# Kernel optimization log

Hardware: AMD Instinct MI355X
Metric: run time of the kernel (lower is better)

## Reference

```python
import jax, jax.numpy as jnp
import numpy as np

# Static config
B, C, H, W = 1, 4, 64, 64
DIM, NH = 512, 16
HD = DIM // NH
SCALE = HD ** -0.5
WC, WH, WW = 2, 8, 8            # 3D window size
N = WC * WH * WW                # tokens per window = 128
SC, SH, SW = 1, 4, 4            # shift = window // 2
NWC, NWH, NWW = C // WC, H // WH, W // WW
NWIN = NWC * NWH * NWW          # windows per sample
HID = 4 * DIM
NBLK = 2                        # [no-shift, shift] pair


def _rel_idx():
    coords = np.stack(np.meshgrid(np.arange(WC), np.arange(WH), np.arange(WW), indexing='ij')).reshape(3, -1)
    rel = coords[:, :, None] - coords[:, None, :]
    rel[0] += WC - 1; rel[1] += WH - 1; rel[2] += WW - 1
    idx = rel[0] * (2 * WH - 1) * (2 * WW - 1) + rel[1] * (2 * WW - 1) + rel[2]
    return jnp.asarray(idx)  # [N, N] into 675-entry table

REL_IDX = _rel_idx()


def _shift_mask():
    img = np.zeros((C, H, W), np.int32)
    cnt = 0
    for cs in (slice(0, -WC), slice(-WC, -SC), slice(-SC, None)):
        for hs in (slice(0, -WH), slice(-WH, -SH), slice(-SH, None)):
            for ws in (slice(0, -WW), slice(-WW, -SW), slice(-SW, None)):
                img[cs, hs, ws] = cnt; cnt += 1
    img = img.reshape(NWC, WC, NWH, WH, NWW, WW).transpose(0, 2, 4, 1, 3, 5).reshape(NWIN, N)
    diff = img[:, :, None] != img[:, None, :]
    return jnp.asarray(np.where(diff, -100.0, 0.0).astype(np.float32))  # [NWIN, N, N]

MASK = _shift_mask()


def _win_part(x):  # [B,C,H,W,D] -> [B*NWIN, N, D]
    x = x.reshape(B, NWC, WC, NWH, WH, NWW, WW, DIM)
    return x.transpose(0, 1, 3, 5, 2, 4, 6, 7).reshape(B * NWIN, N, DIM)


def _win_rev(x):  # [B*NWIN, N, D] -> [B,C,H,W,D]
    x = x.reshape(B, NWC, NWH, NWW, WC, WH, WW, DIM)
    return x.transpose(0, 1, 4, 2, 5, 3, 6, 7).reshape(B, C, H, W, DIM)


def _ln(x, g, b):
    m = x.mean(-1, keepdims=True)
    v = ((x - m) ** 2).mean(-1, keepdims=True)
    return (x - m) / jnp.sqrt(v + 1e-5) * g + b


def _forward(x, ln1_g, ln1_b, qkv_w, qkv_b, bias_tab, proj_w, proj_b,
             ln2_g, ln2_b, fc1_w, fc1_b, fc2_w, fc2_b):
    for i in range(NBLK):
        shifted = (i % 2 == 1)
        shortcut = x
        h = _ln(x, ln1_g[i], ln1_b[i]).reshape(B, C, H, W, DIM)
        if shifted:
            h = jnp.roll(h, (-SC, -SH, -SW), axis=(1, 2, 3))
        xw = _win_part(h)  # [B*NWIN, N, DIM]
        qkv = (xw @ qkv_w[i] + qkv_b[i]).reshape(-1, N, 3, NH, HD).transpose(2, 0, 3, 1, 4)
        q, k, v = qkv[0] * SCALE, qkv[1], qkv[2]       # [B*NWIN, NH, N, HD]
        bias = bias_tab[i][REL_IDX].transpose(2, 0, 1)  # [NH, N, N]
        attn = jnp.einsum('whnd,whmd->whnm', q, k) + bias[None]
        if shifted:
            attn = (attn.reshape(B, NWIN, NH, N, N) + MASK[None, :, None]).reshape(-1, NH, N, N)
        attn = jax.nn.softmax(attn, axis=-1)
        out = jnp.einsum('whnm,whmd->wnhd', attn, v).reshape(-1, N, DIM)
        out = out @ proj_w[i] + proj_b[i]
        h = _win_rev(out)
        if shifted:
            h = jnp.roll(h, (SC, SH, SW), axis=(1, 2, 3))
        x = shortcut + h.reshape(B, C * H * W, DIM)
        h2 = _ln(x, ln2_g[i], ln2_b[i])
        h2 = jax.nn.gelu(h2 @ fc1_w[i] + fc1_b[i], approximate=False) @ fc2_w[i] + fc2_b[i]
        x = x + h2
    return x


def setup_inputs() -> dict:
    key = jax.random.key(0)
    ks = jax.random.split(key, 8)
    s = 0.02
    return {
        'x': jax.random.normal(ks[0], (B, C * H * W, DIM), jnp.float32),
        'ln1_g': jnp.ones((NBLK, DIM), jnp.float32),
        'ln1_b': jnp.zeros((NBLK, DIM), jnp.float32),
        'qkv_w': jax.random.normal(ks[1], (NBLK, DIM, 3 * DIM), jnp.float32) * s,
        'qkv_b': jnp.zeros((NBLK, 3 * DIM), jnp.float32),
        'bias_tab': jax.random.normal(ks[2], (NBLK, (2 * WC - 1) * (2 * WH - 1) * (2 * WW - 1), NH), jnp.float32) * s,
        'proj_w': jax.random.normal(ks[3], (NBLK, DIM, DIM), jnp.float32) * s,
        'proj_b': jnp.zeros((NBLK, DIM), jnp.float32),
        'ln2_g': jnp.ones((NBLK, DIM), jnp.float32),
        'ln2_b': jnp.zeros((NBLK, DIM), jnp.float32),
        'fc1_w': jax.random.normal(ks[4], (NBLK, DIM, HID), jnp.float32) * s,
        'fc1_b': jnp.zeros((NBLK, HID), jnp.float32),
        'fc2_w': jax.random.normal(ks[5], (NBLK, HID, DIM), jnp.float32) * s,
        'fc2_b': jnp.zeros((NBLK, DIM), jnp.float32),
    }


def reference(x, ln1_g, ln1_b, qkv_w, qkv_b, bias_tab, proj_w, proj_b,
              ln2_g, ln2_b, fc1_w, fc1_b, fc2_w, fc2_b):
    return _forward(x, ln1_g, ln1_b, qkv_w, qkv_b, bias_tab, proj_w, proj_b,
                    ln2_g, ln2_b, fc1_w, fc1_b, fc2_w, fc2_b)
```

## Files before the change

kernel.cpp:

```cpp
#include <hip/hip_runtime.h>
#include <stdint.h>

#define DIM 512
#define NHD 16
#define HD 32
#define NTOK 16384

typedef unsigned short u16;
typedef __attribute__((ext_vector_type(8))) short short8;
typedef __attribute__((ext_vector_type(4))) float f32x4;

__device__ __forceinline__ float bf2f(u16 u){ union{unsigned i; float f;} c; c.i=(unsigned)u<<16; return c.f; }
__device__ __forceinline__ float bflo(unsigned u){ union{unsigned i; float f;} c; c.i=u<<16; return c.f; }
__device__ __forceinline__ float bfhi(unsigned u){ union{unsigned i; float f;} c; c.i=u&0xffff0000u; return c.f; }
__device__ __forceinline__ u16 f2bf(float f){ union{float f; unsigned i;} c; c.f=f; unsigned r=(c.i + 0x7fffu + ((c.i>>16)&1u))>>16; return (u16)r; }

__device__ __forceinline__ int win_to_tok(int r, int shifted){
  int win = r >> 7, n = r & 127;
  int a = win >> 6, b = (win >> 3) & 7, c = win & 7;
  int ic = n >> 6, ih = (n >> 3) & 7, iw = n & 7;
  int gc = a*2 + ic, gh = b*8 + ih, gw = c*8 + iw;
  if (shifted){ gc = (gc + 1) & 3; gh = (gh + 4) & 63; gw = (gw + 4) & 63; }
  return (gc << 12) + (gh << 6) + gw;
}

__device__ __forceinline__ void gload16(const void* g, void* l){
  __builtin_amdgcn_global_load_lds(
    (const __attribute__((address_space(1))) unsigned int*)(unsigned long long)g,
    (__attribute__((address_space(3))) unsigned int*)(unsigned int)(unsigned long long)l,
    16, 0, 0);
}

__global__ __launch_bounds__(256)
void transpose_kernel(const float* __restrict__ W, u16* __restrict__ Wt, int K, int N)
{
  __shared__ float t[32][33];
  int n0 = blockIdx.x*32, k0 = blockIdx.y*32;
  int tx = threadIdx.x & 31, ty = threadIdx.x >> 5;
  #pragma unroll
  for (int i=0;i<4;i++) t[ty + i*8][tx] = W[(size_t)(k0 + ty + i*8)*N + n0 + tx];
  __syncthreads();
  #pragma unroll
  for (int i=0;i<4;i++) Wt[(size_t)(n0 + ty + i*8)*K + k0 + tx] = f2bf(t[tx][ty + i*8]);
}

__global__ __launch_bounds__(256)
void ln_kernel(const float* __restrict__ x, const float* __restrict__ g,
               const float* __restrict__ b, u16* __restrict__ out, int mode)
{
  int wave = threadIdx.x >> 6, lane = threadIdx.x & 63;
  int r = blockIdx.x * 4 + wave;
  int src = (mode < 0) ? r : win_to_tok(r, mode);
  const float4* xr = (const float4*)(x + (size_t)src * DIM);
  float4 v0 = xr[lane*2], v1 = xr[lane*2+1];
  float s  = v0.x+v0.y+v0.z+v0.w+v1.x+v1.y+v1.z+v1.w;
  float sq = v0.x*v0.x+v0.y*v0.y+v0.z*v0.z+v0.w*v0.w
           + v1.x*v1.x+v1.y*v1.y+v1.z*v1.z+v1.w*v1.w;
  #pragma unroll
  for (int o=32;o;o>>=1){ s += __shfl_xor(s,o); sq += __shfl_xor(sq,o); }
  float mean = s*(1.f/DIM);
  float var  = sq*(1.f/DIM) - mean*mean;
  float rstd = rsqrtf(var + 1e-5f);
  int c0 = lane*8;
  const float4* g4 = (const float4*)(g + c0);
  const float4* b4 = (const float4*)(b + c0);
  float4 ga = g4[0], gb = g4[1], ba = b4[0], bb = b4[1];
  float xv[8] = {v0.x,v0.y,v0.z,v0.w,v1.x,v1.y,v1.z,v1.w};
  float gg[8] = {ga.x,ga.y,ga.z,ga.w,gb.x,gb.y,gb.z,gb.w};
  float bv[8] = {ba.x,ba.y,ba.z,ba.w,bb.x,bb.y,bb.z,bb.w};
  union{u16 us[8]; uint4 u;} p;
  #pragma unroll
  for (int j=0;j<8;j++) p.us[j] = f2bf((xv[j]-mean)*rstd*gg[j] + bv[j]);
  ((uint4*)(out + (size_t)r*DIM))[lane] = p.u;
}

template<int EPI>
__global__ __launch_bounds__(256)
void gemm_kernel(const u16* __restrict__ X, const u16* __restrict__ Wt,
                 const float* __restrict__ bias, u16* __restrict__ obf,
                 float* __restrict__ xres, int M, int N, int K, int shifted)
{
  __shared__ u16 smem[4][128*64];
  int tid = threadIdx.x, wave = tid>>6, lane = tid&63;
  int nwg = gridDim.x * gridDim.y;
  int bid = blockIdx.y * gridDim.x + blockIdx.x;
  int wg  = (bid & 7) * (nwg >> 3) + (bid >> 3);
  int n0 = (wg % gridDim.x) * 128;
  int m0 = (wg / gridDim.x) * 128;
  int wm = (wave>>1)*64, wn = (wave&1)*64;
  f32x4 acc[4][4] = {};
  int srow = tid>>3;
  int soff = (((tid&7) ^ ((tid>>3)&7)))*8;

  auto stage = [&](int c, int k0){
    #pragma unroll
    for (int i=0;i<4;i++)
      gload16(X + (size_t)(m0 + i*32 + srow)*K + k0 + soff, (void*)(smem[c] + i*2048 + wave*512));
    #pragma unroll
    for (int i=0;i<4;i++)
      gload16(Wt + (size_t)(n0 + i*32 + srow)*K + k0 + soff, (void*)(smem[2+c] + i*2048 + wave*512));
  };

  stage(0, 0);
  __syncthreads();
  int nkt = K >> 6;
  for (int kt=0; kt<nkt; ++kt){
    int c = kt & 1;
    if (kt+1 < nkt) stage(c^1, (kt+1)<<6);
    const u16* Ab = smem[c];
    const u16* Bb = smem[2+c];
    #pragma unroll
    for (int kk=0; kk<64; kk+=32){
      short8 af[4], bfr[4];
      int cofs = (kk + (lane>>4)*8) ^ ((lane&7)<<3);
      #pragma unroll
      for (int mi=0;mi<4;mi++)
        af[mi] = *(const short8*)(Ab + (wm + mi*16 + (lane&15))*64 + cofs);
      #pragma unroll
      for (int nj=0;nj<4;nj++)
        bfr[nj] = *(const short8*)(Bb + (wn + nj*16 + (lane&15))*64 + cofs);
      __builtin_amdgcn_s_setprio(1);
      #pragma unroll
      for (int mi=0;mi<4;mi++)
        #pragma unroll
        for (int nj=0;nj<4;nj++)
          acc[mi][nj] = __builtin_amdgcn_mfma_f32_16x16x32_bf16(af[mi], bfr[nj], acc[mi][nj], 0,0,0);
      __builtin_amdgcn_s_setprio(0);
    }
    __syncthreads();
  }

  int lr = (lane>>4)*4, lc = lane&15;
  if (EPI==0 || EPI==2){
    u16* et = (u16*)smem;
    #pragma unroll
    for (int mi=0;mi<4;mi++){
      #pragma unroll
      for (int nj=0;nj<4;nj++){
        int col = wn + nj*16 + lc;
        float bv = bias[n0 + col];
        #pragma unroll
        for (int rr=0;rr<4;rr++){
          int row = wm + mi*16 + lr + rr;
          float v = acc[mi][nj][rr] + bv;
          if (EPI==2){
            float u2 = v*(1.5957691216057308f + 0.0713548162726f*v*v);
            v = v * __builtin_amdgcn_rcpf(1.f + __expf(-u2));
          }
          *(u16*)((char*)et + ((row*256 + col*2) ^ (((row>>2)&3)<<5))) = f2bf(v);
        }
      }
    }
    __syncthreads();
    #pragma unroll
    for (int j=0;j<8;j++){
      int q = j*256 + tid;
      int row = q>>4, cc = q&15;
      uint4 d = *(const uint4*)((char*)et + ((row*256 + cc*16) ^ (((row>>2)&3)<<5)));
      *(uint4*)(obf + (size_t)(m0+row)*N + n0 + cc*8) = d;
    }
  } else {
    float* et = (float*)smem;
    #pragma unroll
    for (int mi=0;mi<4;mi++){
      #pragma unroll
      for (int nj=0;nj<4;nj++){
        int col = wn + nj*16 + lc;
        float bv = bias[n0 + col];
        #pragma unroll
        for (int rr=0;rr<4;rr++){
          int row = wm + mi*16 + lr + rr;
          *(float*)((char*)et + ((row*512 + col*4) ^ (((row>>2)&1)<<6))) = acc[mi][nj][rr] + bv;
        }
      }
    }
    __syncthreads();
    #pragma unroll
    for (int j=0;j<16;j++){
      int q = j*256 + tid;
      int row = q>>5, cc = q&31;
      float4 d = *(const float4*)((char*)et + ((row*512 + cc*16) ^ (((row>>2)&1)<<6)));
      int grow = (EPI==1) ? win_to_tok(m0+row, shifted) : (m0+row);
      float4* p = (float4*)(xres + (size_t)grow*DIM + n0 + cc*4);
      float4 o = *p;
      o.x += d.x; o.y += d.y; o.z += d.z; o.w += d.w;
      *p = o;
    }
  }
}

__global__ __launch_bounds__(256)
void bias_kernel(const float* __restrict__ btab, float* __restrict__ biasM)
{
  int gid = blockIdx.x*256 + threadIdx.x;
  int q = (gid >> 7) & 127, k = gid & 127, h = gid >> 14;
  int ic=q>>6, ih=(q>>3)&7, iw=q&7, jc=k>>6, jh=(k>>3)&7, jw=k&7;
  int idx = (ic-jc+1)*225 + (ih-jh+7)*15 + (iw-jw+7);
  biasM[gid] = btab[idx*16 + h];
}

__global__ __launch_bounds__(256)
void attn_kernel(const u16* __restrict__ qkv, const float* __restrict__ biasM,
                 u16* __restrict__ out, int shifted)
{
  __shared__ u16 Ks[128*32];
  __shared__ u16 VsT[32*128];
  __shared__ u16 Ps[4][32*128];
  __shared__ int rid[128];
  int win = blockIdx.x >> 4, h = blockIdx.x & 15;
  int tid = threadIdx.x, wave = tid>>6, lane = tid&63;
  size_t base = (size_t)win*128*1536 + (size_t)h*32;

  {
    int m = tid>>1, half = tid&1;
    const uint4* ks = (const uint4*)(qkv + base + (size_t)m*1536 + 512 + half*16);
    uint4 k0v = ks[0], k1v = ks[1];
    char* krow = (char*)Ks + m*64;
    int c0 = half*32, sw = (m&3)<<4;
    *(uint4*)(krow + ((c0     ) ^ sw)) = k0v;
    *(uint4*)(krow + ((c0 + 16) ^ sw)) = k1v;
    const uint4* vs = (const uint4*)(qkv + base + (size_t)m*1536 + 1024 + half*16);
    union{u16 us[16]; uint4 u[2];} vv; vv.u[0]=vs[0]; vv.u[1]=vs[1];
    #pragma unroll
    for (int j=0;j<16;j++){
      int d = half*16 + j;
      *(u16*)((char*)VsT + ((d*256 + m*2) ^ ((d&7)<<4))) = vv.us[j];
    }
  }
  if (shifted && tid < 128){
    int a=win>>6, b=(win>>3)&7, c=win&7;
    int gc=a*2+(tid>>6), gh=b*8+((tid>>3)&7), gw=c*8+(tid&7);
    int rc = (gc<2)?0:((gc<3)?1:2);
    int rh = (gh<56)?0:((gh<60)?1:2);
    int rw = (gw<56)?0:((gw<60)?1:2);
    rid[tid] = rc*9 + rh*3 + rw;
  }
  __syncthreads();

  int q0 = wave*32;
  short8 qf[2];
  #pragma unroll
  for (int mi=0;mi<2;mi++){
    int ql = 16*mi + (lane&15);
    qf[mi] = *(const short8*)(qkv + base + (size_t)(q0+ql)*1536 + (lane>>4)*8);
  }
  f32x4 s[2][8] = {};
  #pragma unroll
  for (int nj=0;nj<8;nj++){
    int row = (lane&15) + 16*nj;
    short8 kf = *(const short8*)((char*)Ks + row*64 + ((((lane>>4)<<4)) ^ ((row&3)<<4)));
    #pragma unroll
    for (int mi=0;mi<2;mi++)
      s[mi][nj] = __builtin_amdgcn_mfma_f32_16x16x32_bf16(qf[mi], kf, s[mi][nj], 0,0,0);
  }

  int rk[8];
  if (shifted){
    #pragma unroll
    for (int nj=0;nj<8;nj++) rk[nj] = rid[(lane&15) + 16*nj];
  }
  float invl[2][4];
  char* pbase = (char*)Ps[wave];
  #pragma unroll
  for (int mi=0;mi<2;mi++){
    #pragma unroll
    for (int r=0;r<4;r++){
      int ql = 16*mi + ((lane>>4)<<2) + r;
      int qw = q0 + ql;
      const float* bp = biasM + (((h<<7) + qw)<<7) + (lane&15);
      int rq = shifted ? rid[qw] : 0;
      float sv[8]; float mx = -1e30f;
      #pragma unroll
      for (int nj=0;nj<8;nj++){
        float v = s[mi][nj][r] * 0.17677669529663687f + bp[nj*16];
        if (shifted && rk[nj] != rq) v -= 100.f;
        sv[nj] = v; mx = fmaxf(mx, v);
      }
      #pragma unroll
      for (int o=1;o<16;o<<=1) mx = fmaxf(mx, __shfl_xor(mx, o));
      float sum = 0.f;
      #pragma unroll
      for (int nj=0;nj<8;nj++){ float p = __expf(sv[nj]-mx); sv[nj]=p; sum += p; }
      #pragma unroll
      for (int o=1;o<16;o<<=1) sum += __shfl_xor(sum, o);
      invl[mi][r] = 1.f/sum;
      char* prow = pbase + ql*256;
      int sw = (ql&7)<<4;
      #pragma unroll
      for (int nj=0;nj<8;nj++)
        *(u16*)(prow + ((((lane&15) + (nj<<4))<<1) ^ sw)) = f2bf(sv[nj]);
    }
  }

  f32x4 o2[2][2] = {};
  #pragma unroll
  for (int kk=0;kk<4;kk++){
    int coff = kk*64 + ((lane>>4)<<4);
    short8 pa[2], vb[2];
    #pragma unroll
    for (int mi=0;mi<2;mi++){
      int ql = 16*mi + (lane&15);
      pa[mi] = *(const short8*)(pbase + ql*256 + (coff ^ ((ql&7)<<4)));
    }
    #pragma unroll
    for (int nj=0;nj<2;nj++){
      int d = (lane&15) + 16*nj;
      vb[nj] = *(const short8*)((char*)VsT + d*256 + (coff ^ ((d&7)<<4)));
    }
    #pragma unroll
    for (int mi=0;mi<2;mi++)
      #pragma unroll
      for (int nj=0;nj<2;nj++)
        o2[mi][nj] = __builtin_amdgcn_mfma_f32_16x16x32_bf16(pa[mi], vb[nj], o2[mi][nj], 0,0,0);
  }

  #pragma unroll
  for (int mi=0;mi<2;mi++){
    #pragma unroll
    for (int nj=0;nj<2;nj++){
      #pragma unroll
      for (int r=0;r<4;r++){
        int ql = 16*mi + ((lane>>4)<<2) + r;
        int d  = (lane&15) + (nj<<4);
        out[(size_t)(win*128 + q0 + ql)*DIM + (h<<5) + d] = f2bf(o2[mi][nj][r] * invl[mi][r]);
      }
    }
  }
}

extern "C" void kernel_launch(void* const* d_in, const int* in_sizes, int n_in,
                              void* d_out, int out_size, void* d_ws, size_t ws_size,
                              hipStream_t stream)
{
  const float* x_in   = (const float*)d_in[0];
  const float* ln1_g  = (const float*)d_in[1];
  const float* ln1_b  = (const float*)d_in[2];
  const float* qkv_w  = (const float*)d_in[3];
  const float* qkv_b  = (const float*)d_in[4];
  const float* btab   = (const float*)d_in[5];
  const float* proj_w = (const float*)d_in[6];
  const float* proj_b = (const float*)d_in[7];
  const float* ln2_g  = (const float*)d_in[8];
  const float* ln2_b  = (const float*)d_in[9];
  const float* fc1_w  = (const float*)d_in[10];
  const float* fc1_b  = (const float*)d_in[11];
  const float* fc2_w  = (const float*)d_in[12];
  const float* fc2_b  = (const float*)d_in[13];

  char* ws = (char*)d_ws;
  size_t off = 0;
  auto alloc = [&](size_t bytes)->char*{ char* p = ws + off; off += (bytes + 255) & ~(size_t)255; return p; };
  u16* wT_qkv = (u16*)alloc((size_t)2*512*1536*2);
  u16* wT_proj= (u16*)alloc((size_t)2*512*512*2);
  u16* wT_fc1 = (u16*)alloc((size_t)2*2048*512*2);
  u16* wT_fc2 = (u16*)alloc((size_t)2*512*2048*2);
  u16* bufA   = (u16*)alloc((size_t)16384*2048*2);
  u16* bufQ   = (u16*)alloc((size_t)16384*1536*2);
  u16* bufB   = (u16*)alloc((size_t)16384*512*2);
  float* biasM= (float*)alloc((size_t)16*128*128*4);
  (void)ws_size; (void)in_sizes; (void)n_in; (void)out_size;

  float* x = (float*)d_out;
  hipMemcpyAsync(x, x_in, (size_t)NTOK*DIM*4, hipMemcpyDeviceToDevice, stream);

  for (int i=0;i<2;i++){
    transpose_kernel<<<dim3(1536/32, 512/32), 256, 0, stream>>>(qkv_w + (size_t)i*512*1536, wT_qkv + (size_t)i*512*1536, 512, 1536);
    transpose_kernel<<<dim3( 512/32, 512/32), 256, 0, stream>>>(proj_w + (size_t)i*512*512,  wT_proj + (size_t)i*512*512,  512, 512);
    transpose_kernel<<<dim3(2048/32, 512/32), 256, 0, stream>>>(fc1_w + (size_t)i*512*2048, wT_fc1 + (size_t)i*2048*512, 512, 2048);
    transpose_kernel<<<dim3( 512/32,2048/32), 256, 0, stream>>>(fc2_w + (size_t)i*2048*512, wT_fc2 + (size_t)i*512*2048, 2048, 512);
  }

  for (int i=0;i<2;i++){
    ln_kernel<<<4096, 256, 0, stream>>>(x, ln1_g+i*512, ln1_b+i*512, bufA, i);
    gemm_kernel<0><<<dim3(12,128), 256, 0, stream>>>(bufA, wT_qkv+(size_t)i*512*1536, qkv_b+i*1536, bufQ, nullptr, NTOK,1536,512, 0);
    bias_kernel<<<1024, 256, 0, stream>>>(btab + (size_t)i*675*16, biasM);
    attn_kernel<<<2048, 256, 0, stream>>>(bufQ, biasM, bufB, i);
    gemm_kernel<1><<<dim3(4,128), 256, 0, stream>>>(bufB, wT_proj+(size_t)i*512*512, proj_b+i*512, nullptr, x, NTOK,512,512, i);
    ln_kernel<<<4096, 256, 0, stream>>>(x, ln2_g+i*512, ln2_b+i*512, bufB, -1);
    gemm_kernel<2><<<dim3(16,128), 256, 0, stream>>>(bufB, wT_fc1+(size_t)i*2048*512, fc1_b+i*2048, bufA, nullptr, NTOK,2048,512, 0);
    gemm_kernel<3><<<dim3(4,128), 256, 0, stream>>>(bufA, wT_fc2+(size_t)i*512*2048, fc2_b+i*512, nullptr, x, NTOK,512,2048, 0);
  }
}
```

Before: 435.8 us.

## Add K=32 GEMM variant with halved LDS for QKV, FC1 and FC2

Adds a gemm32 kernel that stages 32-wide K tiles instead of 64-wide ones. Shared memory drops from 64KB to 32KB, and the LDS layout gets a new XOR swizzle with two rows packed per 128-byte line. The fp32 residual epilogue is split into two 64-row halves so it fits in the smaller buffer. The aim is higher occupancy per CU for the QKV, FC1 and FC2 GEMMs, at the cost of twice as many barriers and K iterations.

```diff
diff --git a/kernel.cpp b/kernel.cpp
--- a/kernel.cpp
+++ b/kernel.cpp
@@ -76,11 +76,11 @@
 
 template<int EPI>
 __global__ __launch_bounds__(256)
-void gemm_kernel(const u16* __restrict__ X, const u16* __restrict__ Wt,
-                 const float* __restrict__ bias, u16* __restrict__ obf,
-                 float* __restrict__ xres, int M, int N, int K, int shifted)
-{
-  __shared__ u16 smem[4][128*64];
+void gemm32_kernel(const u16* __restrict__ X, const u16* __restrict__ Wt,
+                   const float* __restrict__ bias, u16* __restrict__ obf,
+                   float* __restrict__ xres, int M, int N, int K)
+{
+  __shared__ u16 smem[16384];
   int tid = threadIdx.x, wave = tid>>6, lane = tid&63;
   int nwg = gridDim.x * gridDim.y;
   int bid = blockIdx.y * gridDim.x + blockIdx.x;
@@ -89,50 +89,56 @@
   int m0 = (wg / gridDim.x) * 128;
   int wm = (wave>>1)*64, wn = (wave&1)*64;
   f32x4 acc[4][4] = {};
-  int srow = tid>>3;
-  int soff = (((tid&7) ^ ((tid>>3)&7)))*8;
-
-  auto stage = [&](int c, int k0){
-    #pragma unroll
-    for (int i=0;i<4;i++)
-      gload16(X + (size_t)(m0 + i*32 + srow)*K + k0 + soff, (void*)(smem[c] + i*2048 + wave*512));
-    #pragma unroll
-    for (int i=0;i<4;i++)
-      gload16(Wt + (size_t)(n0 + i*32 + srow)*K + k0 + soff, (void*)(smem[2+c] + i*2048 + wave*512));
+
+  int r_[2], c_[2];
+  #pragma unroll
+  for (int q=0;q<2;q++){
+    int line = q*32 + (tid>>3), slot = tid&7;
+    int u = slot ^ (line&7);
+    r_[q] = line*2 + (u>>2); c_[q] = u&3;
+  }
+
+  auto stage = [&](int cs, int kb){
+    u16* Ad = smem + cs*4096;
+    u16* Bd = smem + 8192 + cs*4096;
+    #pragma unroll
+    for (int q=0;q<2;q++){
+      gload16(X + (size_t)(m0 + r_[q])*K + kb + c_[q]*8, (void*)(Ad + q*2048 + tid*8));
+      gload16(Wt + (size_t)(n0 + r_[q])*K + kb + c_[q]*8, (void*)(Bd + q*2048 + tid*8));
+    }
+  };
+  auto ldfrag = [&](const u16* base, int row0)->short8 {
+    int r = row0 + (lane&15);
+    int slot = (((r&1)<<2) + (lane>>4)) ^ ((r>>1)&7);
+    return *(const short8*)((const char*)base + (r>>1)*128 + slot*16);
   };
 
   stage(0, 0);
   __syncthreads();
-  int nkt = K >> 6;
-  for (int kt=0; kt<nkt; ++kt){
-    int c = kt & 1;
-    if (kt+1 < nkt) stage(c^1, (kt+1)<<6);
-    const u16* Ab = smem[c];
-    const u16* Bb = smem[2+c];
-    #pragma unroll
-    for (int kk=0; kk<64; kk+=32){
-      short8 af[4], bfr[4];
-      int cofs = (kk + (lane>>4)*8) ^ ((lane&7)<<3);
-      #pragma unroll
-      for (int mi=0;mi<4;mi++)
-        af[mi] = *(const short8*)(Ab + (wm + mi*16 + (lane&15))*64 + cofs);
+  int nt = K >> 5;
+  for (int t=0; t<nt; ++t){
+    int cs = t & 1;
+    if (t+1 < nt) stage(cs^1, (t+1)<<5);
+    const u16* Ab = smem + cs*4096;
+    const u16* Bb = smem + 8192 + cs*4096;
+    short8 af[4], bfr[4];
+    #pragma unroll
+    for (int mi=0;mi<4;mi++) af[mi]  = ldfrag(Ab, wm + mi*16);
+    #pragma unroll
+    for (int nj=0;nj<4;nj++) bfr[nj] = ldfrag(Bb, wn + nj*16);
+    __builtin_amdgcn_s_setprio(1);
+    #pragma unroll
+    for (int mi=0;mi<4;mi++)
       #pragma unroll
       for (int nj=0;nj<4;nj++)
-        bfr[nj] = *(const short8*)(Bb + (wn + nj*16 + (lane&15))*64 + cofs);
-      __builtin_amdgcn_s_setprio(1);
-      #pragma unroll
-      for (int mi=0;mi<4;mi++)
-        #pragma unroll
-        for (int nj=0;nj<4;nj++)
-          acc[mi][nj] = __builtin_amdgcn_mfma_f32_16x16x32_bf16(af[mi], bfr[nj], acc[mi][nj], 0,0,0);
-      __builtin_amdgcn_s_setprio(0);
-    }
+        acc[mi][nj] = __builtin_amdgcn_mfma_f32_16x16x32_bf16(af[mi], bfr[nj], acc[mi][nj], 0,0,0);
+    __builtin_amdgcn_s_setprio(0);
     __syncthreads();
   }
 
   int lr = (lane>>4)*4, lc = lane&15;
   if (EPI==0 || EPI==2){
-    u16* et = (u16*)smem;
+    u16* et = smem;
     #pragma unroll
     for (int mi=0;mi<4;mi++){
       #pragma unroll
@@ -160,6 +166,98 @@
       *(uint4*)(obf + (size_t)(m0+row)*N + n0 + cc*8) = d;
     }
   } else {
+    float* et = (float*)smem;
+    #pragma unroll
+    for (int half=0; half<2; ++half){
+      __syncthreads();
+      if ((wm>>6) == half){
+        #pragma unroll
+        for (int mi=0;mi<4;mi++){
+          #pragma unroll
+          for (int nj=0;nj<4;nj++){
+            int col = wn + nj*16 + lc;
+            float bv = bias[n0 + col];
+            #pragma unroll
+            for (int rr=0;rr<4;rr++){
+              int row = (wm & 63) + mi*16 + lr + rr;
+              *(float*)((char*)et + ((row*512 + col*4) ^ (((row>>2)&1)<<6))) = acc[mi][nj][rr] + bv;
+            }
+          }
+        }
+      }
+      __syncthreads();
+      #pragma unroll
+      for (int j=0;j<8;j++){
+        int q = j*256 + tid;
+        int row = q>>5, cc = q&31;
+        float4 d = *(const float4*)((char*)et + ((row*512 + cc*16) ^ (((row>>2)&1)<<6)));
+        float4* p = (float4*)(xres + (size_t)(m0 + half*64 + row)*DIM + n0 + cc*4);
+        float4 o = *p;
+        o.x += d.x; o.y += d.y; o.z += d.z; o.w += d.w;
+        *p = o;
+      }
+    }
+  }
+}
+
+template<int EPI>
+__global__ __launch_bounds__(256)
+void gemm_kernel(const u16* __restrict__ X, const u16* __restrict__ Wt,
+                 const float* __restrict__ bias, u16* __restrict__ obf,
+                 float* __restrict__ xres, int M, int N, int K, int shifted)
+{
+  __shared__ u16 smem[4][128*64];
+  int tid = threadIdx.x, wave = tid>>6, lane = tid&63;
+  int nwg = gridDim.x * gridDim.y;
+  int bid = blockIdx.y * gridDim.x + blockIdx.x;
+  int wg  = (bid & 7) * (nwg >> 3) + (bid >> 3);
+  int n0 = (wg % gridDim.x) * 128;
+  int m0 = (wg / gridDim.x) * 128;
+  int wm = (wave>>1)*64, wn = (wave&1)*64;
+  f32x4 acc[4][4] = {};
+  int srow = tid>>3;
+  int soff = (((tid&7) ^ ((tid>>3)&7)))*8;
+
+  auto stage = [&](int c, int k0){
+    #pragma unroll
+    for (int i=0;i<4;i++)
+      gload16(X + (size_t)(m0 + i*32 + srow)*K + k0 + soff, (void*)(smem[c] + i*2048 + wave*512));
+    #pragma unroll
+    for (int i=0;i<4;i++)
+      gload16(Wt + (size_t)(n0 + i*32 + srow)*K + k0 + soff, (void*)(smem[2+c] + i*2048 + wave*512));
+  };
+
+  stage(0, 0);
+  __syncthreads();
+  int nkt = K >> 6;
+  for (int kt=0; kt<nkt; ++kt){
+    int c = kt & 1;
+    if (kt+1 < nkt) stage(c^1, (kt+1)<<6);
+    const u16* Ab = smem[c];
+    const u16* Bb = smem[2+c];
+    #pragma unroll
+    for (int kk=0; kk<64; kk+=32){
+      short8 af[4], bfr[4];
+      int cofs = (kk + (lane>>4)*8) ^ ((lane&7)<<3);
+      #pragma unroll
+      for (int mi=0;mi<4;mi++)
+        af[mi] = *(const short8*)(Ab + (wm + mi*16 + (lane&15))*64 + cofs);
+      #pragma unroll
+      for (int nj=0;nj<4;nj++)
+        bfr[nj] = *(const short8*)(Bb + (wn + nj*16 + (lane&15))*64 + cofs);
+      __builtin_amdgcn_s_setprio(1);
+      #pragma unroll
+      for (int mi=0;mi<4;mi++)
+        #pragma unroll
+        for (int nj=0;nj<4;nj++)
+          acc[mi][nj] = __builtin_amdgcn_mfma_f32_16x16x32_bf16(af[mi], bfr[nj], acc[mi][nj], 0,0,0);
+      __builtin_amdgcn_s_setprio(0);
+    }
+    __syncthreads();
+  }
+
+  int lr = (lane>>4)*4, lc = lane&15;
+  {
     float* et = (float*)smem;
     #pragma unroll
     for (int mi=0;mi<4;mi++){
@@ -372,12 +470,12 @@
 
   for (int i=0;i<2;i++){
     ln_kernel<<<4096, 256, 0, stream>>>(x, ln1_g+i*512, ln1_b+i*512, bufA, i);
-    gemm_kernel<0><<<dim3(12,128), 256, 0, stream>>>(bufA, wT_qkv+(size_t)i*512*1536, qkv_b+i*1536, bufQ, nullptr, NTOK,1536,512, 0);
+    gemm32_kernel<0><<<dim3(12,128), 256, 0, stream>>>(bufA, wT_qkv+(size_t)i*512*1536, qkv_b+i*1536, bufQ, nullptr, NTOK,1536,512);
     bias_kernel<<<1024, 256, 0, stream>>>(btab + (size_t)i*675*16, biasM);
     attn_kernel<<<2048, 256, 0, stream>>>(bufQ, biasM, bufB, i);
     gemm_kernel<1><<<dim3(4,128), 256, 0, stream>>>(bufB, wT_proj+(size_t)i*512*512, proj_b+i*512, nullptr, x, NTOK,512,512, i);
     ln_kernel<<<4096, 256, 0, stream>>>(x, ln2_g+i*512, ln2_b+i*512, bufB, -1);
-    gemm_kernel<2><<<dim3(16,128), 256, 0, stream>>>(bufB, wT_fc1+(size_t)i*2048*512, fc1_b+i*2048, bufA, nullptr, NTOK,2048,512, 0);
-    gemm_kernel<3><<<dim3(4,128), 256, 0, stream>>>(bufA, wT_fc2+(size_t)i*512*2048, fc2_b+i*512, nullptr, x, NTOK,512,2048, 0);
-  }
-}
+    gemm32_kernel<2><<<dim3(16,128), 256, 0, stream>>>(bufB, wT_fc1+(size_t)i*2048*512, fc1_b+i*2048, bufA, nullptr, NTOK,2048,512);
+    gemm32_kernel<3><<<dim3(4,128), 256, 0, stream>>>(bufA, wT_fc2+(size_t)i*512*2048, fc2_b+i*512, nullptr, x, NTOK,512,2048);
+  }
+}
```

Result: slower. 459.3 us (+5.4%).

## Add 256x128-tile GEMM for QKV and FC1, batch weight transposes

Applied to the files above, without the earlier changes.

Adds a new GEMM kernel that uses 256x128 output tiles, BK=32 double buffering and a swizzled LDS layout. It is used for the QKV and FC1 projections, where each wave now computes a 128x64 subtile, to get more operand reuse per LDS fragment load. Weight transposes for both blocks are merged into single launches via blockIdx.z. The cost is more accumulator registers per thread (32 f32x4) and half as many workgroups, which may lower occupancy. The epilogue is also split into two halves through LDS.

```diff
diff --git a/kernel.cpp b/kernel.cpp
--- a/kernel.cpp
+++ b/kernel.cpp
@@ -11,8 +11,6 @@
 typedef __attribute__((ext_vector_type(4))) float f32x4;
 
 __device__ __forceinline__ float bf2f(u16 u){ union{unsigned i; float f;} c; c.i=(unsigned)u<<16; return c.f; }
-__device__ __forceinline__ float bflo(unsigned u){ union{unsigned i; float f;} c; c.i=u<<16; return c.f; }
-__device__ __forceinline__ float bfhi(unsigned u){ union{unsigned i; float f;} c; c.i=u&0xffff0000u; return c.f; }
 __device__ __forceinline__ u16 f2bf(float f){ union{float f; unsigned i;} c; c.f=f; unsigned r=(c.i + 0x7fffu + ((c.i>>16)&1u))>>16; return (u16)r; }
 
 __device__ __forceinline__ int win_to_tok(int r, int shifted){
@@ -35,13 +33,14 @@
 void transpose_kernel(const float* __restrict__ W, u16* __restrict__ Wt, int K, int N)
 {
   __shared__ float t[32][33];
+  size_t zoff = (size_t)blockIdx.z * K * N;
   int n0 = blockIdx.x*32, k0 = blockIdx.y*32;
   int tx = threadIdx.x & 31, ty = threadIdx.x >> 5;
   #pragma unroll
-  for (int i=0;i<4;i++) t[ty + i*8][tx] = W[(size_t)(k0 + ty + i*8)*N + n0 + tx];
+  for (int i=0;i<4;i++) t[ty + i*8][tx] = W[zoff + (size_t)(k0 + ty + i*8)*N + n0 + tx];
   __syncthreads();
   #pragma unroll
-  for (int i=0;i<4;i++) Wt[(size_t)(n0 + ty + i*8)*K + k0 + tx] = f2bf(t[tx][ty + i*8]);
+  for (int i=0;i<4;i++) Wt[zoff + (size_t)(n0 + ty + i*8)*K + k0 + tx] = f2bf(t[tx][ty + i*8]);
 }
 
 __global__ __launch_bounds__(256)
@@ -76,6 +75,105 @@
 
 template<int EPI>
 __global__ __launch_bounds__(256)
+void gemm256_kernel(const u16* __restrict__ X, const u16* __restrict__ Wt,
+                    const float* __restrict__ bias, u16* __restrict__ obf,
+                    int M, int N, int K)
+{
+  __shared__ u16 smem[24576];
+  int tid = threadIdx.x, wave = tid>>6, lane = tid&63;
+  int nwg = gridDim.x * gridDim.y;
+  int bid = blockIdx.y * gridDim.x + blockIdx.x;
+  int wg  = (bid & 7) * (nwg >> 3) + (bid >> 3);
+  int n0 = (wg % gridDim.x) * 128;
+  int m0 = (wg / gridDim.x) * 256;
+  int wm = (wave>>1)*128, wn = (wave&1)*64;
+  f32x4 acc[8][4] = {};
+
+  int rA[4], cA[4];
+  #pragma unroll
+  for (int q=0;q<4;q++){
+    int line = q*32 + (tid>>3), slot = tid&7;
+    int u = slot ^ (line&7);
+    rA[q] = line*2 + (u>>2); cA[q] = u&3;
+  }
+
+  auto stage = [&](int cs, int kb){
+    u16* Ad = smem + cs*12288;
+    u16* Bd = Ad + 8192;
+    #pragma unroll
+    for (int q=0;q<4;q++)
+      gload16(X + (size_t)(m0 + rA[q])*K + kb + cA[q]*8, (void*)(Ad + q*2048 + tid*8));
+    #pragma unroll
+    for (int q=0;q<2;q++)
+      gload16(Wt + (size_t)(n0 + rA[q])*K + kb + cA[q]*8, (void*)(Bd + q*2048 + tid*8));
+  };
+  auto ldfrag = [&](const u16* base, int row0)->short8 {
+    int r = row0 + (lane&15);
+    int slot = (((r&1)<<2) + (lane>>4)) ^ ((r>>1)&7);
+    return *(const short8*)((const char*)base + (r>>1)*128 + slot*16);
+  };
+
+  stage(0, 0);
+  __syncthreads();
+  int nt = K >> 5;
+  for (int t=0; t<nt; ++t){
+    int cs = t & 1;
+    if (t+1 < nt) stage(cs^1, (t+1)<<5);
+    const u16* Ab = smem + cs*12288;
+    const u16* Bb = Ab + 8192;
+    short8 bfr[4];
+    #pragma unroll
+    for (int nj=0;nj<4;nj++) bfr[nj] = ldfrag(Bb, wn + nj*16);
+    #pragma unroll
+    for (int mi=0;mi<8;mi++){
+      short8 af = ldfrag(Ab, wm + mi*16);
+      __builtin_amdgcn_s_setprio(1);
+      #pragma unroll
+      for (int nj=0;nj<4;nj++)
+        acc[mi][nj] = __builtin_amdgcn_mfma_f32_16x16x32_bf16(af, bfr[nj], acc[mi][nj], 0,0,0);
+      __builtin_amdgcn_s_setprio(0);
+    }
+    __syncthreads();
+  }
+
+  int lr = (lane>>4)*4, lc = lane&15;
+  u16* et = smem;
+  #pragma unroll
+  for (int half=0; half<2; ++half){
+    if ((wm>>7) == half){
+      #pragma unroll
+      for (int mi=0;mi<8;mi++){
+        #pragma unroll
+        for (int nj=0;nj<4;nj++){
+          int col = wn + nj*16 + lc;
+          float bv = bias[n0 + col];
+          #pragma unroll
+          for (int rr=0;rr<4;rr++){
+            int row = (wm&127) + mi*16 + lr + rr;
+            float v = acc[mi][nj][rr] + bv;
+            if (EPI==2){
+              float u2 = v*(1.5957691216057308f + 0.0713548162726f*v*v);
+              v = v * __builtin_amdgcn_rcpf(1.f + __expf(-u2));
+            }
+            *(u16*)((char*)et + ((row*256 + col*2) ^ (((row>>2)&3)<<5))) = f2bf(v);
+          }
+        }
+      }
+    }
+    __syncthreads();
+    #pragma unroll
+    for (int j=0;j<8;j++){
+      int q = j*256 + tid;
+      int row = q>>4, cc = q&15;
+      uint4 d = *(const uint4*)((char*)et + ((row*256 + cc*16) ^ (((row>>2)&3)<<5)));
+      *(uint4*)(obf + (size_t)(m0 + half*128 + row)*N + n0 + cc*8) = d;
+    }
+    __syncthreads();
+  }
+}
+
+template<int EPI>
+__global__ __launch_bounds__(256)
 void gemm_kernel(const u16* __restrict__ X, const u16* __restrict__ Wt,
                  const float* __restrict__ bias, u16* __restrict__ obf,
                  float* __restrict__ xres, int M, int N, int K, int shifted)
@@ -131,35 +229,7 @@
   }
 
   int lr = (lane>>4)*4, lc = lane&15;
-  if (EPI==0 || EPI==2){
-    u16* et = (u16*)smem;
-    #pragma unroll
-    for (int mi=0;mi<4;mi++){
-      #pragma unroll
-      for (int nj=0;nj<4;nj++){
-        int col = wn + nj*16 + lc;
-        float bv = bias[n0 + col];
-        #pragma unroll
-        for (int rr=0;rr<4;rr++){
-          int row = wm + mi*16 + lr + rr;
-          float v = acc[mi][nj][rr] + bv;
-          if (EPI==2){
-            float u2 = v*(1.5957691216057308f + 0.0713548162726f*v*v);
-            v = v * __builtin_amdgcn_rcpf(1.f + __expf(-u2));
-          }
-          *(u16*)((char*)et + ((row*256 + col*2) ^ (((row>>2)&3)<<5))) = f2bf(v);
-        }
-      }
-    }
-    __syncthreads();
-    #pragma unroll
-    for (int j=0;j<8;j++){
-      int q = j*256 + tid;
-      int row = q>>4, cc = q&15;
-      uint4 d = *(const uint4*)((char*)et + ((row*256 + cc*16) ^ (((row>>2)&3)<<5)));
-      *(uint4*)(obf + (size_t)(m0+row)*N + n0 + cc*8) = d;
-    }
-  } else {
+  {
     float* et = (float*)smem;
     #pragma unroll
     for (int mi=0;mi<4;mi++){
@@ -363,21 +433,19 @@
   float* x = (float*)d_out;
   hipMemcpyAsync(x, x_in, (size_t)NTOK*DIM*4, hipMemcpyDeviceToDevice, stream);
 
-  for (int i=0;i<2;i++){
-    transpose_kernel<<<dim3(1536/32, 512/32), 256, 0, stream>>>(qkv_w + (size_t)i*512*1536, wT_qkv + (size_t)i*512*1536, 512, 1536);
-    transpose_kernel<<<dim3( 512/32, 512/32), 256, 0, stream>>>(proj_w + (size_t)i*512*512,  wT_proj + (size_t)i*512*512,  512, 512);
-    transpose_kernel<<<dim3(2048/32, 512/32), 256, 0, stream>>>(fc1_w + (size_t)i*512*2048, wT_fc1 + (size_t)i*2048*512, 512, 2048);
-    transpose_kernel<<<dim3( 512/32,2048/32), 256, 0, stream>>>(fc2_w + (size_t)i*2048*512, wT_fc2 + (size_t)i*512*2048, 2048, 512);
-  }
+  transpose_kernel<<<dim3(1536/32, 512/32, 2), 256, 0, stream>>>(qkv_w, wT_qkv, 512, 1536);
+  transpose_kernel<<<dim3( 512/32, 512/32, 2), 256, 0, stream>>>(proj_w, wT_proj, 512, 512);
+  transpose_kernel<<<dim3(2048/32, 512/32, 2), 256, 0, stream>>>(fc1_w, wT_fc1, 512, 2048);
+  transpose_kernel<<<dim3( 512/32,2048/32, 2), 256, 0, stream>>>(fc2_w, wT_fc2, 2048, 512);
 
   for (int i=0;i<2;i++){
     ln_kernel<<<4096, 256, 0, stream>>>(x, ln1_g+i*512, ln1_b+i*512, bufA, i);
-    gemm_kernel<0><<<dim3(12,128), 256, 0, stream>>>(bufA, wT_qkv+(size_t)i*512*1536, qkv_b+i*1536, bufQ, nullptr, NTOK,1536,512, 0);
+    gemm256_kernel<0><<<dim3(12,64), 256, 0, stream>>>(bufA, wT_qkv+(size_t)i*512*1536, qkv_b+i*1536, bufQ, NTOK,1536,512);
     bias_kernel<<<1024, 256, 0, stream>>>(btab + (size_t)i*675*16, biasM);
     attn_kernel<<<2048, 256, 0, stream>>>(bufQ, biasM, bufB, i);
     gemm_kernel<1><<<dim3(4,128), 256, 0, stream>>>(bufB, wT_proj+(size_t)i*512*512, proj_b+i*512, nullptr, x, NTOK,512,512, i);
     ln_kernel<<<4096, 256, 0, stream>>>(x, ln2_g+i*512, ln2_b+i*512, bufB, -1);
-    gemm_kernel<2><<<dim3(16,128), 256, 0, stream>>>(bufB, wT_fc1+(size_t)i*2048*512, fc1_b+i*2048, bufA, nullptr, NTOK,2048,512, 0);
+    gemm256_kernel<2><<<dim3(16,64), 256, 0, stream>>>(bufB, wT_fc1+(size_t)i*2048*512, fc1_b+i*2048, bufA, NTOK,2048,512);
     gemm_kernel<3><<<dim3(4,128), 256, 0, stream>>>(bufA, wT_fc2+(size_t)i*512*2048, fc2_b+i*512, nullptr, x, NTOK,512,2048, 0);
   }
 }
```

Result: slower. 548.2 us (+25.8%).

## Use 3-stage K=32 LDS pipeline in GEMM with split-barrier waits

Applied to the files above, without the earlier changes.

The GEMM main loop moves from a double-buffered K=64 tile to a triple-buffered K=32 tile with a new swizzled LDS layout. It uses explicit vmcnt/lgkmcnt waits and a single s_barrier per iteration, so loads run two stages ahead. Shared memory drops from 64KB to 48KB, which may allow more workgroups per CU; to fit, the fp32 residual epilogue is done in two 64-row halves. The weight transpose launches are also merged into one launch per weight using a z-dimension. The cost is more loop iterations and barriers per K, plus hand-tuned wait counts that must exactly match the number of outstanding loads.

```diff
diff --git a/kernel.cpp b/kernel.cpp
--- a/kernel.cpp
+++ b/kernel.cpp
@@ -11,8 +11,6 @@
 typedef __attribute__((ext_vector_type(4))) float f32x4;
 
 __device__ __forceinline__ float bf2f(u16 u){ union{unsigned i; float f;} c; c.i=(unsigned)u<<16; return c.f; }
-__device__ __forceinline__ float bflo(unsigned u){ union{unsigned i; float f;} c; c.i=u<<16; return c.f; }
-__device__ __forceinline__ float bfhi(unsigned u){ union{unsigned i; float f;} c; c.i=u&0xffff0000u; return c.f; }
 __device__ __forceinline__ u16 f2bf(float f){ union{float f; unsigned i;} c; c.f=f; unsigned r=(c.i + 0x7fffu + ((c.i>>16)&1u))>>16; return (u16)r; }
 
 __device__ __forceinline__ int win_to_tok(int r, int shifted){
@@ -35,13 +33,14 @@
 void transpose_kernel(const float* __restrict__ W, u16* __restrict__ Wt, int K, int N)
 {
   __shared__ float t[32][33];
+  size_t zoff = (size_t)blockIdx.z * K * N;
   int n0 = blockIdx.x*32, k0 = blockIdx.y*32;
   int tx = threadIdx.x & 31, ty = threadIdx.x >> 5;
   #pragma unroll
-  for (int i=0;i<4;i++) t[ty + i*8][tx] = W[(size_t)(k0 + ty + i*8)*N + n0 + tx];
+  for (int i=0;i<4;i++) t[ty + i*8][tx] = W[zoff + (size_t)(k0 + ty + i*8)*N + n0 + tx];
   __syncthreads();
   #pragma unroll
-  for (int i=0;i<4;i++) Wt[(size_t)(n0 + ty + i*8)*K + k0 + tx] = f2bf(t[tx][ty + i*8]);
+  for (int i=0;i<4;i++) Wt[zoff + (size_t)(n0 + ty + i*8)*K + k0 + tx] = f2bf(t[tx][ty + i*8]);
 }
 
 __global__ __launch_bounds__(256)
@@ -76,11 +75,11 @@
 
 template<int EPI>
 __global__ __launch_bounds__(256)
-void gemm_kernel(const u16* __restrict__ X, const u16* __restrict__ Wt,
-                 const float* __restrict__ bias, u16* __restrict__ obf,
-                 float* __restrict__ xres, int M, int N, int K, int shifted)
-{
-  __shared__ u16 smem[4][128*64];
+void gemm32r_kernel(const u16* __restrict__ X, const u16* __restrict__ Wt,
+                    const float* __restrict__ bias, u16* __restrict__ obf,
+                    float* __restrict__ xres, int M, int N, int K, int shifted)
+{
+  __shared__ u16 smem[24576];
   int tid = threadIdx.x, wave = tid>>6, lane = tid&63;
   int nwg = gridDim.x * gridDim.y;
   int bid = blockIdx.y * gridDim.x + blockIdx.x;
@@ -89,50 +88,70 @@
   int m0 = (wg / gridDim.x) * 128;
   int wm = (wave>>1)*64, wn = (wave&1)*64;
   f32x4 acc[4][4] = {};
-  int srow = tid>>3;
-  int soff = (((tid&7) ^ ((tid>>3)&7)))*8;
-
-  auto stage = [&](int c, int k0){
-    #pragma unroll
-    for (int i=0;i<4;i++)
-      gload16(X + (size_t)(m0 + i*32 + srow)*K + k0 + soff, (void*)(smem[c] + i*2048 + wave*512));
-    #pragma unroll
-    for (int i=0;i<4;i++)
-      gload16(Wt + (size_t)(n0 + i*32 + srow)*K + k0 + soff, (void*)(smem[2+c] + i*2048 + wave*512));
+
+  int r_[2], c_[2];
+  #pragma unroll
+  for (int q=0;q<2;q++){
+    int line = q*32 + (tid>>3), slot = tid&7;
+    int u = slot ^ (line&7);
+    r_[q] = line*2 + (u>>2); c_[q] = u&3;
+  }
+
+  auto stage = [&](int s, int kb){
+    u16* Ad = smem + s*4096;
+    u16* Bd = smem + 12288 + s*4096;
+    #pragma unroll
+    for (int q=0;q<2;q++){
+      gload16(X + (size_t)(m0 + r_[q])*K + kb + c_[q]*8, (void*)(Ad + q*2048 + tid*8));
+      gload16(Wt + (size_t)(n0 + r_[q])*K + kb + c_[q]*8, (void*)(Bd + q*2048 + tid*8));
+    }
   };
-
-  stage(0, 0);
-  __syncthreads();
-  int nkt = K >> 6;
-  for (int kt=0; kt<nkt; ++kt){
-    int c = kt & 1;
-    if (kt+1 < nkt) stage(c^1, (kt+1)<<6);
-    const u16* Ab = smem[c];
-    const u16* Bb = smem[2+c];
-    #pragma unroll
-    for (int kk=0; kk<64; kk+=32){
-      short8 af[4], bfr[4];
-      int cofs = (kk + (lane>>4)*8) ^ ((lane&7)<<3);
-      #pragma unroll
-      for (int mi=0;mi<4;mi++)
-        af[mi] = *(const short8*)(Ab + (wm + mi*16 + (lane&15))*64 + cofs);
+  auto ldfrag = [&](const u16* base, int row0)->short8 {
+    int r = row0 + (lane&15);
+    int slot = (((r&1)<<2) + (lane>>4)) ^ ((r>>1)&7);
+    return *(const short8*)((const char*)base + (r>>1)*128 + slot*16);
+  };
+
+  int nt = K >> 5;
+  stage(0, 0); stage(1, 32);
+  asm volatile("s_waitcnt vmcnt(4)" ::: "memory");
+  __builtin_amdgcn_sched_barrier(0);
+  __builtin_amdgcn_s_barrier();
+  __builtin_amdgcn_sched_barrier(0);
+
+  int s = 0;
+  for (int t=0; t<nt; ++t){
+    int s2 = s+2; if (s2>=3) s2-=3;
+    if (t+2 < nt) stage(s2, (t+2)<<5);
+    const u16* Ab = smem + s*4096;
+    const u16* Bb = smem + 12288 + s*4096;
+    short8 af[4], bfr[4];
+    #pragma unroll
+    for (int mi=0;mi<4;mi++) af[mi]  = ldfrag(Ab, wm + mi*16);
+    #pragma unroll
+    for (int nj=0;nj<4;nj++) bfr[nj] = ldfrag(Bb, wn + nj*16);
+    __builtin_amdgcn_s_setprio(1);
+    #pragma unroll
+    for (int mi=0;mi<4;mi++)
       #pragma unroll
       for (int nj=0;nj<4;nj++)
-        bfr[nj] = *(const short8*)(Bb + (wn + nj*16 + (lane&15))*64 + cofs);
-      __builtin_amdgcn_s_setprio(1);
-      #pragma unroll
-      for (int mi=0;mi<4;mi++)
-        #pragma unroll
-        for (int nj=0;nj<4;nj++)
-          acc[mi][nj] = __builtin_amdgcn_mfma_f32_16x16x32_bf16(af[mi], bfr[nj], acc[mi][nj], 0,0,0);
-      __builtin_amdgcn_s_setprio(0);
-    }
-    __syncthreads();
+        acc[mi][nj] = __builtin_amdgcn_mfma_f32_16x16x32_bf16(af[mi], bfr[nj], acc[mi][nj], 0,0,0);
+    __builtin_amdgcn_s_setprio(0);
+    asm volatile("s_waitcnt lgkmcnt(0)" ::: "memory");
+    __builtin_amdgcn_sched_barrier(0);
+    if (t+1 < nt){
+      if (t+2 < nt) asm volatile("s_waitcnt vmcnt(4)" ::: "memory");
+      else          asm volatile("s_waitcnt vmcnt(0)" ::: "memory");
+      __builtin_amdgcn_sched_barrier(0);
+    }
+    __builtin_amdgcn_s_barrier();
+    __builtin_amdgcn_sched_barrier(0);
+    s = (s==2) ? 0 : s+1;
   }
 
   int lr = (lane>>4)*4, lc = lane&15;
   if (EPI==0 || EPI==2){
-    u16* et = (u16*)smem;
+    u16* et = smem;
     #pragma unroll
     for (int mi=0;mi<4;mi++){
       #pragma unroll
@@ -162,29 +181,35 @@
   } else {
     float* et = (float*)smem;
     #pragma unroll
-    for (int mi=0;mi<4;mi++){
-      #pragma unroll
-      for (int nj=0;nj<4;nj++){
-        int col = wn + nj*16 + lc;
-        float bv = bias[n0 + col];
+    for (int half=0; half<2; ++half){
+      __syncthreads();
+      if ((wm>>6) == half){
         #pragma unroll
-        for (int rr=0;rr<4;rr++){
-          int row = wm + mi*16 + lr + rr;
-          *(float*)((char*)et + ((row*512 + col*4) ^ (((row>>2)&1)<<6))) = acc[mi][nj][rr] + bv;
+        for (int mi=0;mi<4;mi++){
+          #pragma unroll
+          for (int nj=0;nj<4;nj++){
+            int col = wn + nj*16 + lc;
+            float bv = bias[n0 + col];
+            #pragma unroll
+            for (int rr=0;rr<4;rr++){
+              int row = (wm & 63) + mi*16 + lr + rr;
+              *(float*)((char*)et + ((row*512 + col*4) ^ (((row>>2)&1)<<6))) = acc[mi][nj][rr] + bv;
+            }
+          }
         }
       }
-    }
-    __syncthreads();
-    #pragma unroll
-    for (int j=0;j<16;j++){
-      int q = j*256 + tid;
-      int row = q>>5, cc = q&31;
-      float4 d = *(const float4*)((char*)et + ((row*512 + cc*16) ^ (((row>>2)&1)<<6)));
-      int grow = (EPI==1) ? win_to_tok(m0+row, shifted) : (m0+row);
-      float4* p = (float4*)(xres + (size_t)grow*DIM + n0 + cc*4);
-      float4 o = *p;
-      o.x += d.x; o.y += d.y; o.z += d.z; o.w += d.w;
-      *p = o;
+      __syncthreads();
+      #pragma unroll
+      for (int j=0;j<8;j++){
+        int q = j*256 + tid;
+        int row = q>>5, cc = q&31;
+        float4 d = *(const float4*)((char*)et + ((row*512 + cc*16) ^ (((row>>2)&1)<<6)));
+        int grow = (EPI==1) ? win_to_tok(m0 + half*64 + row, shifted) : (m0 + half*64 + row);
+        float4* p = (float4*)(xres + (size_t)grow*DIM + n0 + cc*4);
+        float4 o = *p;
+        o.x += d.x; o.y += d.y; o.z += d.z; o.w += d.w;
+        *p = o;
+      }
     }
   }
 }
@@ -363,21 +388,19 @@
   float* x = (float*)d_out;
   hipMemcpyAsync(x, x_in, (size_t)NTOK*DIM*4, hipMemcpyDeviceToDevice, stream);
 
-  for (int i=0;i<2;i++){
-    transpose_kernel<<<dim3(1536/32, 512/32), 256, 0, stream>>>(qkv_w + (size_t)i*512*1536, wT_qkv + (size_t)i*512*1536, 512, 1536);
-    transpose_kernel<<<dim3( 512/32, 512/32), 256, 0, stream>>>(proj_w + (size_t)i*512*512,  wT_proj + (size_t)i*512*512,  512, 512);
-    transpose_kernel<<<dim3(2048/32, 512/32), 256, 0, stream>>>(fc1_w + (size_t)i*512*2048, wT_fc1 + (size_t)i*2048*512, 512, 2048);
-    transpose_kernel<<<dim3( 512/32,2048/32), 256, 0, stream>>>(fc2_w + (size_t)i*2048*512, wT_fc2 + (size_t)i*512*2048, 2048, 512);
-  }
+  transpose_kernel<<<dim3(1536/32, 512/32, 2), 256, 0, stream>>>(qkv_w, wT_qkv, 512, 1536);
+  transpose_kernel<<<dim3( 512/32, 512/32, 2), 256, 0, stream>>>(proj_w, wT_proj, 512, 512);
+  transpose_kernel<<<dim3(2048/32, 512/32, 2), 256, 0, stream>>>(fc1_w, wT_fc1, 512, 2048);
+  transpose_kernel<<<dim3( 512/32,2048/32, 2), 256, 0, stream>>>(fc2_w, wT_fc2, 2048, 512);
 
   for (int i=0;i<2;i++){
     ln_kernel<<<4096, 256, 0, stream>>>(x, ln1_g+i*512, ln1_b+i*512, bufA, i);
-    gemm_kernel<0><<<dim3(12,128), 256, 0, stream>>>(bufA, wT_qkv+(size_t)i*512*1536, qkv_b+i*1536, bufQ, nullptr, NTOK,1536,512, 0);
+    gemm32r_kernel<0><<<dim3(12,128), 256, 0, stream>>>(bufA, wT_qkv+(size_t)i*512*1536, qkv_b+i*1536, bufQ, nullptr, NTOK,1536,512, 0);
     bias_kernel<<<1024, 256, 0, stream>>>(btab + (size_t)i*675*16, biasM);
     attn_kernel<<<2048, 256, 0, stream>>>(bufQ, biasM, bufB, i);
-    gemm_kernel<1><<<dim3(4,128), 256, 0, stream>>>(bufB, wT_proj+(size_t)i*512*512, proj_b+i*512, nullptr, x, NTOK,512,512, i);
+    gemm32r_kernel<1><<<dim3(4,128), 256, 0, stream>>>(bufB, wT_proj+(size_t)i*512*512, proj_b+i*512, nullptr, x, NTOK,512,512, i);
     ln_kernel<<<4096, 256, 0, stream>>>(x, ln2_g+i*512, ln2_b+i*512, bufB, -1);
-    gemm_kernel<2><<<dim3(16,128), 256, 0, stream>>>(bufB, wT_fc1+(size_t)i*2048*512, fc1_b+i*2048, bufA, nullptr, NTOK,2048,512, 0);
-    gemm_kernel<3><<<dim3(4,128), 256, 0, stream>>>(bufA, wT_fc2+(size_t)i*512*2048, fc2_b+i*512, nullptr, x, NTOK,512,2048, 0);
-  }
-}
+    gemm32r_kernel<2><<<dim3(16,128), 256, 0, stream>>>(bufB, wT_fc1+(size_t)i*2048*512, fc1_b+i*2048, bufA, nullptr, NTOK,2048,512, 0);
+    gemm32r_kernel<3><<<dim3(4,128), 256, 0, stream>>>(bufA, wT_fc2+(size_t)i*512*2048, fc2_b+i*512, nullptr, x, NTOK,512,2048, 0);
+  }
+}
```

After: 449.8 us. 3.2% more time.
